# Optimization experiments

Measured on AMD Instinct MI355X. Metric: run time of the kernel, lower is better.

Reference implementation:

```python
import jax, jax.numpy as jnp
import numpy as np

B, S, D, U = 32, 4096, 512, 128

def setup_inputs() -> dict:
    key = jax.random.key(0)
    k1, k2, k3, k4, k5 = jax.random.split(key, 5)
    query = jax.random.normal(k1, (B, D), dtype=jnp.float32)
    values = jax.random.normal(k2, (B, S, D), dtype=jnp.float32)
    s = 1.0 / np.sqrt(D)
    W1 = jax.random.normal(k3, (D, U), dtype=jnp.float32) * s
    W2 = jax.random.normal(k4, (D, U), dtype=jnp.float32) * s
    V = jax.random.normal(k5, (U, 1), dtype=jnp.float32) * (1.0 / np.sqrt(U))
    b1 = jnp.zeros((U,), dtype=jnp.float32)
    b2 = jnp.zeros((U,), dtype=jnp.float32)
    bv = jnp.zeros((1,), dtype=jnp.float32)
    return {"query": query, "values": values, "W1": W1, "b1": b1,
            "W2": W2, "b2": b2, "V": V, "bv": bv}

def reference(query, values, W1, b1, W2, b2, V, bv):
    # query: [B, D] -> [B, 1, U]; values: [B, S, D] -> [B, S, U]
    q_proj = (query @ W1 + b1)[:, None, :]                  # [B, 1, U]
    v_proj = jnp.einsum('bsd,du->bsu', values, W2) + b2      # [B, S, U]
    score = jnp.tanh(q_proj + v_proj) @ V + bv               # [B, S, 1]
    attention_weights = jax.nn.softmax(score, axis=1)        # [B, S, 1]
    context_vector = jnp.sum(attention_weights * values, axis=1)  # [B, D]
    return context_vector, attention_weights
```

## Files before the change

### kernel.cpp

```cpp
#include <hip/hip_runtime.h>
#include <math.h>

#define NB 32
#define NS 4096
#define ND 512
#define NU 128

typedef __bf16 bf16x8 __attribute__((ext_vector_type(8)));
typedef unsigned short u16x8 __attribute__((ext_vector_type(8)));
typedef float f32x4 __attribute__((ext_vector_type(4)));

union FragCvt { u16x8 u; bf16x8 b; };

__device__ inline unsigned short f2bf(float x) {
  union { float f; unsigned u; } v; v.f = x;
  return (unsigned short)((v.u + 0x7FFFu + ((v.u >> 16) & 1u)) >> 16);
}
__device__ inline float fast_tanh(float x) {
  x = fminf(9.f, fmaxf(-9.f, x));
  float e2 = __expf(2.f * x);
  return (e2 - 1.f) * __builtin_amdgcn_rcpf(e2 + 1.f);
}
__device__ inline int bswz(int byte) { return byte ^ (((byte >> 7) & 7) << 4); }

__global__ void prep_qb(const float* __restrict__ q, const float* __restrict__ W1,
                        const float* __restrict__ b1, const float* __restrict__ b2,
                        float* __restrict__ qb) {
  const int bb = blockIdx.x >> 4;
  const int kc = blockIdx.x & 15;
  const int u  = threadIdx.x & 127;
  const int dh = threadIdx.x >> 7;
  const int d0 = kc * 32 + dh * 16;
  const float* qr = q + bb * ND + d0;
  const float* w  = W1 + (size_t)d0 * NU + u;
  float s = (kc == 0 && dh == 0) ? (b1[u] + b2[u]) : 0.f;
  #pragma unroll
  for (int j = 0; j < 16; ++j) s += qr[j] * w[j * NU];
  atomicAdd(qb + bb * NU + u, s);
}

__global__ void prep_w2s(const float* __restrict__ W2, unsigned short* __restrict__ w2s) {
  const int idx = blockIdx.x * 256 + threadIdx.x;
  const int u = idx & 127;
  const int r = idx >> 7;
  const int k = r & 31, kt = r >> 5;
  w2s[kt * 4096 + u * 32 + k] = f2bf(W2[(size_t)(kt * 32 + k) * NU + u]);
}

__global__ __launch_bounds__(512, 1) void fused_attn(
    const float* __restrict__ values,
    const float* __restrict__ qb,
    const unsigned short* __restrict__ w2s,
    const float* __restrict__ V,
    const float* __restrict__ bvp,
    float* __restrict__ wout,
    float* __restrict__ Cacc,
    float* __restrict__ Lacc)
{
  __shared__ unsigned short Bs[16 * 4096];
  __shared__ float e_lds[2][128];

  const int tid = threadIdx.x;
  const int blk = blockIdx.x;
  const int b = blk >> 4;
  const int pair = blk & 15;

  const uint4* w2s4 = (const uint4*)w2s;
  #pragma unroll
  for (int i = 0; i < 16; ++i) {
    const int m = i * 512 + tid;
    const uint4 v = w2s4[m];
    *(uint4*)((char*)Bs + (m >> 9) * 8192 + bswz((m & 511) * 16)) = v;
  }
  __syncthreads();

  const int wave = tid >> 6, lane = tid & 63;
  const int quad = lane >> 4, lidx = lane & 15;

  int boff[8];
  #pragma unroll
  for (int nt = 0; nt < 8; ++nt)
    boff[nt] = bswz((nt * 16 + lidx) * 64 + quad * 16);

  float qv[8], vv[8];
  #pragma unroll
  for (int nt = 0; nt < 8; ++nt) {
    qv[nt] = qb[b * NU + nt * 16 + lidx];
    vv[nt] = V[nt * 16 + lidx];
  }
  const float bv = *bvp;

  for (int c = 0; c < 2; ++c) {
    const int s0c = (pair * 2 + c) * 128;
    const int row = s0c + wave * 16 + lidx;
    const float* abase = values + ((size_t)b * NS + row) * ND + quad * 8;

    f32x4 acc[8] = {{0.f,0.f,0.f,0.f},{0.f,0.f,0.f,0.f},{0.f,0.f,0.f,0.f},{0.f,0.f,0.f,0.f},
                    {0.f,0.f,0.f,0.f},{0.f,0.f,0.f,0.f},{0.f,0.f,0.f,0.f},{0.f,0.f,0.f,0.f}};
    #pragma unroll 4
    for (int kt = 0; kt < 16; ++kt) {
      const float4 a0 = *(const float4*)(abase + kt * 32);
      const float4 a1 = *(const float4*)(abase + kt * 32 + 4);
      FragCvt a;
      a.b[0] = (__bf16)a0.x; a.b[1] = (__bf16)a0.y;
      a.b[2] = (__bf16)a0.z; a.b[3] = (__bf16)a0.w;
      a.b[4] = (__bf16)a1.x; a.b[5] = (__bf16)a1.y;
      a.b[6] = (__bf16)a1.z; a.b[7] = (__bf16)a1.w;
      const char* bt = (const char*)Bs + kt * 8192;
      #pragma unroll
      for (int nt = 0; nt < 8; ++nt) {
        FragCvt bf; bf.u = *(const u16x8*)(bt + boff[nt]);
        acc[nt] = __builtin_amdgcn_mfma_f32_16x16x32_bf16(a.b, bf.b, acc[nt], 0, 0, 0);
      }
    }

    float part[4] = {0.f, 0.f, 0.f, 0.f};
    #pragma unroll
    for (int nt = 0; nt < 8; ++nt) {
      #pragma unroll
      for (int r = 0; r < 4; ++r)
        part[r] += fast_tanh(acc[nt][r] + qv[nt]) * vv[nt];
    }
    #pragma unroll
    for (int m = 1; m <= 8; m <<= 1) {
      #pragma unroll
      for (int r = 0; r < 4; ++r) part[r] += __shfl_xor(part[r], m, 64);
    }
    const int r3 = lidx & 3;
    float tmp = (r3 == 0) ? part[0] : (r3 == 1) ? part[1] : (r3 == 2) ? part[2] : part[3];
    const float sc = __shfl(tmp, (lidx >> 2) * 16 + lidx, 64);
    const float e = __expf(sc + bv);
    if (quad == 0) {
      wout[(size_t)b * NS + s0c + wave * 16 + lidx] = e;
      e_lds[c][wave * 16 + lidx] = e;
    }
    float es = e;
    es += __shfl_xor(es, 1, 64); es += __shfl_xor(es, 2, 64);
    es += __shfl_xor(es, 4, 64); es += __shfl_xor(es, 8, 64);
    if (lane == 0) atomicAdd(Lacc + b, es);

    __syncthreads();

    const float* vcol = values + ((size_t)b * NS + s0c) * ND + tid;
    float csum = 0.f;
    #pragma unroll 8
    for (int r = 0; r < 128; ++r)
      csum += e_lds[c][r] * vcol[(size_t)r * ND];
    atomicAdd(Cacc + b * ND + tid, csum);
  }
}

__global__ void finalize(const float* __restrict__ Cacc, const float* __restrict__ Lacc,
                         float* __restrict__ out) {
  int idx = blockIdx.x * 256 + threadIdx.x;
  if (idx < NB * ND) {
    int b = idx >> 9;
    out[idx] = Cacc[idx] / Lacc[b];
  } else {
    int j = idx - NB * ND;
    int b = j >> 12;
    out[idx] = out[idx] / Lacc[b];
  }
}

extern "C" void kernel_launch(void* const* d_in, const int* in_sizes, int n_in,
                              void* d_out, int out_size, void* d_ws, size_t ws_size,
                              hipStream_t stream) {
  const float* query  = (const float*)d_in[0];
  const float* values = (const float*)d_in[1];
  const float* W1     = (const float*)d_in[2];
  const float* b1     = (const float*)d_in[3];
  const float* W2     = (const float*)d_in[4];
  const float* b2     = (const float*)d_in[5];
  const float* V      = (const float*)d_in[6];
  const float* bv     = (const float*)d_in[7];
  float* out = (float*)d_out;

  char* ws = (char*)d_ws;
  float* Cacc = (float*)ws;
  float* Lacc = (float*)(ws + 65536);
  float* qb   = (float*)(ws + 66048);
  unsigned short* w2s = (unsigned short*)(ws + 66048 + 16384);

  hipMemsetAsync(ws, 0, 66048 + 16384, stream);

  prep_qb <<<NB * 16, 256, 0, stream>>>(query, W1, b1, b2, qb);
  prep_w2s<<<256, 256, 0, stream>>>(W2, w2s);
  fused_attn<<<512, 512, 0, stream>>>(values, qb, w2s, V, bv,
                                      out + NB * ND, Cacc, Lacc);
  finalize<<<(NB * ND + NB * NS) / 256, 256, 0, stream>>>(Cacc, Lacc, out);
}
```

Baseline: 451.2 us.

## Use 1024-thread blocks with two halves sharing W2 LDS; vectorize context pass

```diff
diff --git a/kernel.cpp b/kernel.cpp
--- a/kernel.cpp
+++ b/kernel.cpp
@@ -47,7 +47,7 @@
   w2s[kt * 4096 + u * 32 + k] = f2bf(W2[(size_t)(kt * 32 + k) * NU + u]);
 }
 
-__global__ __launch_bounds__(512, 1) void fused_attn(
+__global__ __launch_bounds__(1024, 1) void fused_attn(
     const float* __restrict__ values,
     const float* __restrict__ qb,
     const unsigned short* __restrict__ w2s,
@@ -58,17 +58,17 @@
     float* __restrict__ Lacc)
 {
   __shared__ unsigned short Bs[16 * 4096];
-  __shared__ float e_lds[2][128];
+  __shared__ float e_lds[2][2][128];
 
   const int tid = threadIdx.x;
   const int blk = blockIdx.x;
-  const int b = blk >> 4;
-  const int pair = blk & 15;
+  const int b = blk >> 3;
+  const int eighth = blk & 7;
 
   const uint4* w2s4 = (const uint4*)w2s;
   #pragma unroll
-  for (int i = 0; i < 16; ++i) {
-    const int m = i * 512 + tid;
+  for (int i = 0; i < 8; ++i) {
+    const int m = i * 1024 + tid;
     const uint4 v = w2s4[m];
     *(uint4*)((char*)Bs + (m >> 9) * 8192 + bswz((m & 511) * 16)) = v;
   }
@@ -76,6 +76,8 @@
 
   const int wave = tid >> 6, lane = tid & 63;
   const int quad = lane >> 4, lidx = lane & 15;
+  const int h = wave >> 3;
+  const int wl = wave & 7;
 
   int boff[8];
   #pragma unroll
@@ -91,8 +93,9 @@
   const float bv = *bvp;
 
   for (int c = 0; c < 2; ++c) {
-    const int s0c = (pair * 2 + c) * 128;
-    const int row = s0c + wave * 16 + lidx;
+    const int chunk = eighth * 4 + h * 2 + c;
+    const int s0c = chunk * 128;
+    const int row = s0c + wl * 16 + lidx;
     const float* abase = values + ((size_t)b * NS + row) * ND + quad * 8;
 
     f32x4 acc[8] = {{0.f,0.f,0.f,0.f},{0.f,0.f,0.f,0.f},{0.f,0.f,0.f,0.f},{0.f,0.f,0.f,0.f},
@@ -131,8 +134,8 @@
     const float sc = __shfl(tmp, (lidx >> 2) * 16 + lidx, 64);
     const float e = __expf(sc + bv);
     if (quad == 0) {
-      wout[(size_t)b * NS + s0c + wave * 16 + lidx] = e;
-      e_lds[c][wave * 16 + lidx] = e;
+      wout[(size_t)b * NS + s0c + wl * 16 + lidx] = e;
+      e_lds[h][c][wl * 16 + lidx] = e;
     }
     float es = e;
     es += __shfl_xor(es, 1, 64); es += __shfl_xor(es, 2, 64);
@@ -141,12 +144,20 @@
 
     __syncthreads();
 
-    const float* vcol = values + ((size_t)b * NS + s0c) * ND + tid;
-    float csum = 0.f;
+    const int col4 = tid & 127;
+    const int rg = (tid >> 7) & 3;
+    const float* vb = values + ((size_t)b * NS + s0c + rg * 32) * ND + col4 * 4;
+    float4 cs = {0.f, 0.f, 0.f, 0.f};
     #pragma unroll 8
-    for (int r = 0; r < 128; ++r)
-      csum += e_lds[c][r] * vcol[(size_t)r * ND];
-    atomicAdd(Cacc + b * ND + tid, csum);
+    for (int r = 0; r < 32; ++r) {
+      const float w = e_lds[h][c][rg * 32 + r];
+      const float4 v = *(const float4*)(vb + (size_t)r * ND);
+      cs.x += w * v.x; cs.y += w * v.y; cs.z += w * v.z; cs.w += w * v.w;
+    }
+    atomicAdd(Cacc + b * ND + col4 * 4 + 0, cs.x);
+    atomicAdd(Cacc + b * ND + col4 * 4 + 1, cs.y);
+    atomicAdd(Cacc + b * ND + col4 * 4 + 2, cs.z);
+    atomicAdd(Cacc + b * ND + col4 * 4 + 3, cs.w);
   }
 }
 
@@ -186,7 +197,7 @@
 
   prep_qb <<<NB * 16, 256, 0, stream>>>(query, W1, b1, b2, qb);
   prep_w2s<<<256, 256, 0, stream>>>(W2, w2s);
-  fused_attn<<<512, 512, 0, stream>>>(values, qb, w2s, V, bv,
-                                      out + NB * ND, Cacc, Lacc);
+  fused_attn<<<NB * 8, 1024, 0, stream>>>(values, qb, w2s, V, bv,
+                                          out + NB * ND, Cacc, Lacc);
   finalize<<<(NB * ND + NB * NS) / 256, 256, 0, stream>>>(Cacc, Lacc, out);
 }
```

Measured after the change: 443.2 us. Within noise of the previous version (-1.8%).
